# Kernel tuning notes

Hardware: AMD Instinct MI355X
Metric: run time of the kernel (lower is better)

## Reference

```python
import jax, jax.numpy as jnp
from jax import lax
import numpy as np

H = 768          # x_position_dim = num_atoms*3
L = 10           # num_layers
W = 10           # window_size
B = 512          # batch (number of windows)
N_ATOMS = 256


def setup_inputs() -> dict:
    key = jax.random.key(0)
    ks = jax.random.split(key, 9)
    s = 0.02
    return {
        "x_position": jax.random.normal(ks[0], (B, W, N_ATOMS, 3), jnp.float32),
        "fc0_w": jax.random.normal(ks[1], (H, H), jnp.float32) * s,
        "fc0_b": jax.random.normal(ks[2], (H,), jnp.float32) * s,
        "w_ih": jax.random.normal(ks[3], (L, 4 * H, H), jnp.float32) * s,
        "w_hh": jax.random.normal(ks[4], (L, 4 * H, H), jnp.float32) * s,
        "b_ih": jax.random.normal(ks[5], (L, 4 * H), jnp.float32) * s,
        "b_hh": jax.random.normal(ks[6], (L, 4 * H), jnp.float32) * s,
        "fc1_w": jax.random.normal(ks[7], (H, H * W), jnp.float32) * s,
        "fc1_b": jax.random.normal(ks[8], (H,), jnp.float32) * s,
    }


def _lstm_layer(x, wih, whh, bih, bhh):
    # x: (T, B, H). PyTorch gate order: i, f, g, o.
    T, Bb, Hh = x.shape
    # precompute input contribution for all timesteps (one big GEMM)
    gx = jnp.einsum('tbh,gh->tbg', x, wih) + bih + bhh  # (T, B, 4H)

    def step(carry, g_t):
        h, c = carry
        g = g_t + h @ whh.T  # (B, 4H)
        i, f, gg, o = jnp.split(g, 4, axis=-1)
        i = jax.nn.sigmoid(i)
        f = jax.nn.sigmoid(f)
        gg = jnp.tanh(gg)
        o = jax.nn.sigmoid(o)
        c = f * c + i * gg
        h = o * jnp.tanh(c)
        return (h, c), h

    h0 = jnp.zeros((Bb, Hh), x.dtype)
    _, ys = lax.scan(step, (h0, h0), gx)
    return ys  # (T, B, H)


def reference(x_position, fc0_w, fc0_b, w_ih, w_hh, b_ih, b_hh, fc1_w, fc1_b):
    # reshape (B, W, N, 3) -> (B, W, H) -> (W, B, H)
    x = x_position.reshape(-1, W, H)
    x = jnp.swapaxes(x, 0, 1)
    x = x @ fc0_w.T + fc0_b  # fc0
    for l in range(L):
        x = _lstm_layer(x, w_ih[l], w_hh[l], b_ih[l], b_hh[l])
    # (W, B, H) -> (B, W*H) -> fc1 -> (-1, 3)
    xx = jnp.swapaxes(x, 0, 1).reshape(-1, H * W)
    out = xx @ fc1_w.T + fc1_b  # (B, H)
    return out.reshape(-1, 3)
```

## Files before the change

### kernel.cpp

```cpp
#include <hip/hip_runtime.h>

namespace {

using u16 = unsigned short;
typedef short s16x8 __attribute__((ext_vector_type(8)));
typedef float f32x4 __attribute__((ext_vector_type(4)));
typedef u16 u16x4 __attribute__((ext_vector_type(4)));

constexpr int kH  = 768;
constexpr int kW  = 10;
constexpr int kL  = 10;
constexpr int kB  = 512;
constexpr int kG  = 3072;
constexpr int kTB = 5120;
constexpr int kFC1_SPLIT = 12;

__device__ __forceinline__ u16 f2bf(float x) {
  unsigned u = __float_as_uint(x);
  unsigned r = (u + 0x7fffu + ((u >> 16) & 1u)) >> 16;
  return (u16)r;
}
__device__ __forceinline__ float bf2f(u16 h) {
  return __uint_as_float(((unsigned)h) << 16);
}

__device__ __forceinline__ void gl2lds(const void* g, void* l) {
  __builtin_amdgcn_global_load_lds(
      (const __attribute__((address_space(1))) void*)g,
      (__attribute__((address_space(3))) void*)l, 16, 0, 0);
}

__device__ __forceinline__ f32x4 mfma16(s16x8 a, s16x8 b, f32x4 c) {
  return __builtin_amdgcn_mfma_f32_16x16x32_bf16(a, b, c, 0, 0, 0);
}

__device__ __forceinline__ float sigm(float x) { return 1.f / (1.f + __expf(-x)); }

__device__ __forceinline__ int swz_u16(int row, int kc) {
  return row * 32 + ((kc ^ ((row >> 1) & 3)) << 3);
}

__device__ __forceinline__ void split_store(const float4 v, u16* hi, u16* lo, int idx) {
  u16x4 h, l;
  h[0] = f2bf(v.x); l[0] = f2bf(v.x - bf2f(h[0]));
  h[1] = f2bf(v.y); l[1] = f2bf(v.y - bf2f(h[1]));
  h[2] = f2bf(v.z); l[2] = f2bf(v.z - bf2f(h[2]));
  h[3] = f2bf(v.w); l[3] = f2bf(v.w - bf2f(h[3]));
  reinterpret_cast<u16x4*>(hi)[idx] = h;
  reinterpret_cast<u16x4*>(lo)[idx] = l;
}

__global__ __launch_bounds__(256) void split4(const float* __restrict__ in,
                                              u16* __restrict__ hi,
                                              u16* __restrict__ lo) {
  int idx = blockIdx.x * 256 + threadIdx.x;
  split_store(reinterpret_cast<const float4*>(in)[idx], hi, lo, idx);
}

__global__ __launch_bounds__(256) void split2(const float* __restrict__ a,
                                              const float* __restrict__ b,
                                              u16* __restrict__ ahi, u16* __restrict__ alo,
                                              u16* __restrict__ bhi, u16* __restrict__ blo) {
  int idx = blockIdx.x * 256 + threadIdx.x;
  constexpr int half = kG * kH / 4;
  const float* in = a;
  u16 *hi = ahi, *lo = alo;
  if (idx >= half) { in = b; hi = bhi; lo = blo; idx -= half; }
  split_store(reinterpret_cast<const float4*>(in)[idx], hi, lo, idx);
}

__global__ __launch_bounds__(256) void transpose_split(const float* __restrict__ src,
                                                       u16* __restrict__ hi,
                                                       u16* __restrict__ lo) {
  int idx = blockIdx.x * 256 + threadIdx.x;
  int h4 = idx % 192;
  int rest = idx / 192;
  int b = rest % kB;
  int t = rest / kB;
  float4 v = reinterpret_cast<const float4*>(src)[((size_t)b * kW + t) * 192 + h4];
  split_store(v, hi, lo, (int)(((size_t)t * kB + b) * 192 + h4));
}

__global__ __launch_bounds__(256) void pack_sp(const u16* __restrict__ Yhi,
                                               const u16* __restrict__ Ylo,
                                               u16* __restrict__ Xhi,
                                               u16* __restrict__ Xlo) {
  int idx = blockIdx.x * 256 + threadIdx.x;
  int h8 = idx % 96;
  int rest = idx / 96;
  int w = rest % kW;
  int b = rest / kW;
  size_t s = ((size_t)w * kB + b) * 96 + h8;
  size_t d = ((size_t)b * kW + w) * 96 + h8;
  reinterpret_cast<uint4*>(Xhi)[d] = reinterpret_cast<const uint4*>(Yhi)[s];
  reinterpret_cast<uint4*>(Xlo)[d] = reinterpret_cast<const uint4*>(Ylo)[s];
}

template <int BM, int EPI>
__global__ __launch_bounds__(256) void gemm_bf3(
    const u16* __restrict__ Ahi, const u16* __restrict__ Alo,
    const u16* __restrict__ Bhi, const u16* __restrict__ Blo,
    const float* __restrict__ bias1, const float* __restrict__ bias2,
    float* __restrict__ Cf, u16* __restrict__ Chi, u16* __restrict__ Clo,
    int M, int N, int K, int Ksub) {
  constexpr int MR = BM / 64;
  constexpr int WR = BM / 4;
  __shared__ u16 sAh[2][BM * 32], sAl[2][BM * 32];
  __shared__ u16 sBh[2][128 * 32], sBl[2][128 * 32];
  const int tid = threadIdx.x;
  const int wid = tid >> 6;
  const int lane = tid & 63;
  const int bm = blockIdx.y * BM;
  const int bn = blockIdx.x * 128;
  const int kbeg = blockIdx.z * Ksub;

  f32x4 acc[MR][8];
#pragma unroll
  for (int m = 0; m < MR; ++m)
#pragma unroll
    for (int n = 0; n < 8; ++n) acc[m][n] = {0.f, 0.f, 0.f, 0.f};

  const int kc = lane >> 4;
  const int cl = lane & 15;
  const int srow = lane >> 2;
  const int scol = (((lane & 3) ^ ((srow >> 1) & 3)) << 3);

  auto STAGE = [&](int bi, int k0) {
#pragma unroll
    for (int c = 0; c < MR; ++c) {
      int g16 = (wid * MR + c) * 16;
      size_t goff = (size_t)(bm + g16 + srow) * K + k0 + scol;
      gl2lds(Ahi + goff, &sAh[bi][g16 * 32]);
      gl2lds(Alo + goff, &sAl[bi][g16 * 32]);
    }
#pragma unroll
    for (int c = 0; c < 2; ++c) {
      int g16 = (wid * 2 + c) * 16;
      size_t goff = (size_t)(bn + g16 + srow) * K + k0 + scol;
      gl2lds(Bhi + goff, &sBh[bi][g16 * 32]);
      gl2lds(Blo + goff, &sBl[bi][g16 * 32]);
    }
  };

  auto COMPUTE = [&](int bi) {
    s16x8 ah[MR], al[MR];
#pragma unroll
    for (int m = 0; m < MR; ++m) {
      int row = wid * WR + m * 16 + cl;
      ah[m] = *reinterpret_cast<const s16x8*>(&sAh[bi][swz_u16(row, kc)]);
      al[m] = *reinterpret_cast<const s16x8*>(&sAl[bi][swz_u16(row, kc)]);
    }
#pragma unroll
    for (int n = 0; n < 8; ++n) {
      int row = n * 16 + cl;
      s16x8 bh = *reinterpret_cast<const s16x8*>(&sBh[bi][swz_u16(row, kc)]);
      s16x8 bl = *reinterpret_cast<const s16x8*>(&sBl[bi][swz_u16(row, kc)]);
#pragma unroll
      for (int m = 0; m < MR; ++m) acc[m][n] = mfma16(ah[m], bh, acc[m][n]);
#pragma unroll
      for (int m = 0; m < MR; ++m) acc[m][n] = mfma16(ah[m], bl, acc[m][n]);
#pragma unroll
      for (int m = 0; m < MR; ++m) acc[m][n] = mfma16(al[m], bh, acc[m][n]);
    }
  };

  const int NT = Ksub / 32;
  STAGE(0, kbeg);
  int cur = 0;
  for (int t = 0; t < NT - 1; ++t) {
    STAGE(cur ^ 1, kbeg + (t + 1) * 32);
    if constexpr (MR == 2) asm volatile("s_waitcnt vmcnt(8)" ::: "memory");
    else                   asm volatile("s_waitcnt vmcnt(6)" ::: "memory");
    __builtin_amdgcn_s_barrier();
    __builtin_amdgcn_sched_barrier(0);
    COMPUTE(cur);
    __builtin_amdgcn_sched_barrier(0);
    __builtin_amdgcn_s_barrier();
    cur ^= 1;
  }
  asm volatile("s_waitcnt vmcnt(0)" ::: "memory");
  __builtin_amdgcn_s_barrier();
  __builtin_amdgcn_sched_barrier(0);
  COMPUTE(cur);

  const int rq = (lane >> 4) * 4;
#pragma unroll
  for (int m = 0; m < MR; ++m) {
#pragma unroll
    for (int n = 0; n < 8; ++n) {
      int col = bn + n * 16 + cl;
      float badd = (EPI != 3 && bias1) ? bias1[col] : 0.f;
      if (EPI == 2) badd += bias2[col];
#pragma unroll
      for (int q = 0; q < 4; ++q) {
        int row = bm + wid * WR + m * 16 + rq + q;
        float v = acc[m][n][q] + badd;
        if (EPI == 1) {
          size_t off = (size_t)row * N + col;
          u16 h = f2bf(v);
          Chi[off] = h;
          Clo[off] = f2bf(v - bf2f(h));
        } else if (EPI == 3) {
          size_t off = ((size_t)blockIdx.z * M + row) * N + col;
          Cf[off] = v;
        } else {
          Cf[(size_t)row * N + col] = v;
        }
      }
    }
  }
}

__global__ __launch_bounds__(256) void fc1_reduce(const float* __restrict__ part,
                                                  const float* __restrict__ bias,
                                                  float* __restrict__ out) {
  int idx = blockIdx.x * 256 + threadIdx.x;
  float s = bias[idx % kH];
#pragma unroll
  for (int z = 0; z < kFC1_SPLIT; ++z) s += part[(size_t)z * kB * kH + idx];
  out[idx] = s;
}

__global__ __launch_bounds__(256) void lstm_step(
    const u16* __restrict__ Hhi, const u16* __restrict__ Hlo,
    const u16* __restrict__ Whi, const u16* __restrict__ Wlo,
    const float* __restrict__ gxt,
    float* __restrict__ cbuf,
    u16* __restrict__ Ohi, u16* __restrict__ Olo) {
  __shared__ u16 sAh[2][64 * 32], sAl[2][64 * 32];
  __shared__ u16 sBh[2][128 * 32], sBl[2][128 * 32];
  const int tid = threadIdx.x;
  const int wid = tid >> 6;
  const int lane = tid & 63;
  const int u0 = blockIdx.x * 32;
  const int bm = blockIdx.y * 64;

  f32x4 acc[8];
#pragma unroll
  for (int n = 0; n < 8; ++n) acc[n] = {0.f, 0.f, 0.f, 0.f};

  const int kc = lane >> 4;
  const int cl = lane & 15;
  const int srow = lane >> 2;
  const int scol = (((lane & 3) ^ ((srow >> 1) & 3)) << 3);

  auto STAGE = [&](int bi, int k0) {
    {
      int g16 = wid * 16;
      size_t goff = (size_t)(bm + g16 + srow) * kH + k0 + scol;
      gl2lds(Hhi + goff, &sAh[bi][g16 * 32]);
      gl2lds(Hlo + goff, &sAl[bi][g16 * 32]);
    }
#pragma unroll
    for (int c = 0; c < 2; ++c) {
      int g16 = (wid * 2 + c) * 16;
      int slab = g16 >> 5;
      int jb = g16 & 31;
      size_t goff = (size_t)(slab * kH + u0 + jb + srow) * kH + k0 + scol;
      gl2lds(Whi + goff, &sBh[bi][g16 * 32]);
      gl2lds(Wlo + goff, &sBl[bi][g16 * 32]);
    }
  };

  auto COMPUTE = [&](int bi) {
    int arow = wid * 16 + cl;
    s16x8 ah = *reinterpret_cast<const s16x8*>(&sAh[bi][swz_u16(arow, kc)]);
    s16x8 al = *reinterpret_cast<const s16x8*>(&sAl[bi][swz_u16(arow, kc)]);
#pragma unroll
    for (int n = 0; n < 8; ++n) {
      int row = n * 16 + cl;
      s16x8 bh = *reinterpret_cast<const s16x8*>(&sBh[bi][swz_u16(row, kc)]);
      s16x8 bl = *reinterpret_cast<const s16x8*>(&sBl[bi][swz_u16(row, kc)]);
      acc[n] = mfma16(ah, bh, acc[n]);
      acc[n] = mfma16(ah, bl, acc[n]);
      acc[n] = mfma16(al, bh, acc[n]);
    }
  };

  constexpr int NT = kH / 32;
  STAGE(0, 0);
  int cur = 0;
  for (int t = 0; t < NT - 1; ++t) {
    STAGE(cur ^ 1, (t + 1) * 32);
    asm volatile("s_waitcnt vmcnt(6)" ::: "memory");
    __builtin_amdgcn_s_barrier();
    __builtin_amdgcn_sched_barrier(0);
    COMPUTE(cur);
    __builtin_amdgcn_sched_barrier(0);
    __builtin_amdgcn_s_barrier();
    cur ^= 1;
  }
  asm volatile("s_waitcnt vmcnt(0)" ::: "memory");
  __builtin_amdgcn_s_barrier();
  __builtin_amdgcn_sched_barrier(0);
  COMPUTE(cur);

  const int rq = (lane >> 4) * 4;
#pragma unroll
  for (int h = 0; h < 2; ++h) {
    int u = u0 + h * 16 + cl;
#pragma unroll
    for (int q = 0; q < 4; ++q) {
      int r = bm + wid * 16 + rq + q;
      size_t gb = (size_t)r * kG;
      float gi = acc[0 + h][q] + gxt[gb + u];
      float gf = acc[2 + h][q] + gxt[gb + kH + u];
      float gg = acc[4 + h][q] + gxt[gb + 2 * kH + u];
      float go = acc[6 + h][q] + gxt[gb + 3 * kH + u];
      float i_ = sigm(gi), f_ = sigm(gf), g_ = tanhf(gg), o_ = sigm(go);
      size_t co = (size_t)r * kH + u;
      float cn = fmaf(f_, cbuf[co], i_ * g_);
      cbuf[co] = cn;
      float hv = o_ * tanhf(cn);
      u16 hh = f2bf(hv);
      Ohi[co] = hh;
      Olo[co] = f2bf(hv - bf2f(hh));
    }
  }
}

__global__ __launch_bounds__(256) void lstm_t0(const float* __restrict__ gxt,
                                               float* __restrict__ cbuf,
                                               u16* __restrict__ Ohi,
                                               u16* __restrict__ Olo) {
  int idx = blockIdx.x * 256 + threadIdx.x;
  int b = idx / kH, u = idx % kH;
  size_t base = (size_t)b * kG;
  float gi = gxt[base + u];
  float gg = gxt[base + 2 * kH + u];
  float go = gxt[base + 3 * kH + u];
  float i_ = sigm(gi), g_ = tanhf(gg), o_ = sigm(go);
  float cn = i_ * g_;
  cbuf[idx] = cn;
  float hv = o_ * tanhf(cn);
  u16 hh = f2bf(hv);
  Ohi[idx] = hh;
  Olo[idx] = f2bf(hv - bf2f(hh));
}

}

extern "C" void kernel_launch(void* const* d_in, const int* in_sizes, int n_in,
                              void* d_out, int out_size, void* d_ws, size_t ws_size,
                              hipStream_t stream) {
  const float* xpos  = (const float*)d_in[0];
  const float* fc0_w = (const float*)d_in[1];
  const float* fc0_b = (const float*)d_in[2];
  const float* w_ih  = (const float*)d_in[3];
  const float* w_hh  = (const float*)d_in[4];
  const float* b_ih  = (const float*)d_in[5];
  const float* b_hh  = (const float*)d_in[6];
  const float* fc1_w = (const float*)d_in[7];
  const float* fc1_b = (const float*)d_in[8];
  float* out = (float*)d_out;

  char* W = (char*)d_ws;
  float* gx      = (float*)W;
  u16* Xthi      = (u16*)W;
  u16* Xtlo      = Xthi + (size_t)kTB * kH;
  u16* fc1whi    = (u16*)(W + 16777216);
  u16* fc1wlo    = fc1whi + (size_t)kH * kH * kW;
  float* fc1part = (float*)(W + 40370176);
  u16* Yhi       = (u16*)(W + 62914560);
  u16* Ylo       = Yhi + (size_t)kTB * kH;
  float* cbuf    = (float*)(W + 78643200);
  u16* wihhi     = (u16*)(W + 80216064);
  u16* wihlo     = wihhi + (size_t)kG * kH;
  u16* whhhi     = (u16*)(W + 89653248);
  u16* whhlo     = whhhi + (size_t)kG * kH;
  u16* fc0whi    = (u16*)(W + 99090432);
  u16* fc0wlo    = fc0whi + (size_t)kH * kH;

  dim3 blk(256);

  transpose_split<<<3840, blk, 0, stream>>>(xpos, Xthi, Xtlo);
  split4<<<576, blk, 0, stream>>>(fc0_w, fc0whi, fc0wlo);

  gemm_bf3<128, 1><<<dim3(6, 40), blk, 0, stream>>>(
      Xthi, Xtlo, fc0whi, fc0wlo, fc0_b, nullptr, nullptr, Yhi, Ylo,
      kTB, kH, kH, kH);

  for (int l = 0; l < kL; ++l) {
    split2<<<4608, blk, 0, stream>>>(w_ih + (size_t)l * kG * kH,
                                     w_hh + (size_t)l * kG * kH,
                                     wihhi, wihlo, whhhi, whhlo);

    gemm_bf3<128, 2><<<dim3(24, 40), blk, 0, stream>>>(
        Yhi, Ylo, wihhi, wihlo, b_ih + (size_t)l * kG, b_hh + (size_t)l * kG,
        gx, nullptr, nullptr, kTB, kG, kH, kH);

    lstm_t0<<<1536, blk, 0, stream>>>(gx, cbuf, Yhi, Ylo);

    for (int t = 1; t < kW; ++t) {
      lstm_step<<<dim3(24, 8), blk, 0, stream>>>(
          Yhi + (size_t)(t - 1) * kB * kH, Ylo + (size_t)(t - 1) * kB * kH,
          whhhi, whhlo, gx + (size_t)t * kB * kG, cbuf,
          Yhi + (size_t)t * kB * kH, Ylo + (size_t)t * kB * kH);
    }
  }

  split4<<<5760, blk, 0, stream>>>(fc1_w, fc1whi, fc1wlo);
  pack_sp<<<1920, blk, 0, stream>>>(Yhi, Ylo, Xthi, Xtlo);
  gemm_bf3<64, 3><<<dim3(6, 8, kFC1_SPLIT), blk, 0, stream>>>(
      Xthi, Xtlo, fc1whi, fc1wlo, nullptr, nullptr, fc1part, nullptr, nullptr,
      kB, kH, kW * kH, kW * kH / kFC1_SPLIT);
  fc1_reduce<<<1536, blk, 0, stream>>>(fc1part, fc1_b, out);
}
```

Baseline: 3.604 ms.

## Run stacked LSTM as a layer-time wavefront with fused input and recurrent GEMMs

Replaces the per-layer schedule (weight split, big input GEMM, then nine sequential step kernels) with 19 diagonal wavefront launches. Each launch computes every (layer, time) cell on one anti-diagonal, so up to ten layers run concurrently and fill the GPU better. Each cell fuses the input projection and the recurrent projection into a single 48-tile K loop. The fp32 weights are read directly and split into bf16 hi/lo inside the kernel with packed converts, which removes the separate split kernels and the gx buffer. The cost is re-reading and re-converting both weight matrices in every cell instead of once per layer, and the t=0 cells still skip the recurrent half.

```diff
diff --git a/kernel.cpp b/kernel.cpp
--- a/kernel.cpp
+++ b/kernel.cpp
@@ -22,6 +22,11 @@
 }
 __device__ __forceinline__ float bf2f(u16 h) {
   return __uint_as_float(((unsigned)h) << 16);
+}
+__device__ __forceinline__ unsigned cvtpk(float a, float b) {
+  unsigned r;
+  asm("v_cvt_pk_bf16_f32 %0, %1, %2" : "=v"(r) : "v"(a), "v"(b));
+  return r;
 }
 
 __device__ __forceinline__ void gl2lds(const void* g, void* l) {
@@ -54,18 +59,6 @@
                                               u16* __restrict__ hi,
                                               u16* __restrict__ lo) {
   int idx = blockIdx.x * 256 + threadIdx.x;
-  split_store(reinterpret_cast<const float4*>(in)[idx], hi, lo, idx);
-}
-
-__global__ __launch_bounds__(256) void split2(const float* __restrict__ a,
-                                              const float* __restrict__ b,
-                                              u16* __restrict__ ahi, u16* __restrict__ alo,
-                                              u16* __restrict__ bhi, u16* __restrict__ blo) {
-  int idx = blockIdx.x * 256 + threadIdx.x;
-  constexpr int half = kG * kH / 4;
-  const float* in = a;
-  u16 *hi = ahi, *lo = alo;
-  if (idx >= half) { in = b; hi = bhi; lo = blo; idx -= half; }
   split_store(reinterpret_cast<const float4*>(in)[idx], hi, lo, idx);
 }
 
@@ -100,7 +93,7 @@
 __global__ __launch_bounds__(256) void gemm_bf3(
     const u16* __restrict__ Ahi, const u16* __restrict__ Alo,
     const u16* __restrict__ Bhi, const u16* __restrict__ Blo,
-    const float* __restrict__ bias1, const float* __restrict__ bias2,
+    const float* __restrict__ bias1,
     float* __restrict__ Cf, u16* __restrict__ Chi, u16* __restrict__ Clo,
     int M, int N, int K, int Ksub) {
   constexpr int MR = BM / 64;
@@ -190,7 +183,6 @@
     for (int n = 0; n < 8; ++n) {
       int col = bn + n * 16 + cl;
       float badd = (EPI != 3 && bias1) ? bias1[col] : 0.f;
-      if (EPI == 2) badd += bias2[col];
 #pragma unroll
       for (int q = 0; q < 4; ++q) {
         int row = bm + wid * WR + m * 16 + rq + q;
@@ -200,11 +192,9 @@
           u16 h = f2bf(v);
           Chi[off] = h;
           Clo[off] = f2bf(v - bf2f(h));
-        } else if (EPI == 3) {
+        } else {
           size_t off = ((size_t)blockIdx.z * M + row) * N + col;
           Cf[off] = v;
-        } else {
-          Cf[(size_t)row * N + col] = v;
         }
       }
     }
@@ -221,44 +211,88 @@
   out[idx] = s;
 }
 
-__global__ __launch_bounds__(256) void lstm_step(
-    const u16* __restrict__ Hhi, const u16* __restrict__ Hlo,
-    const u16* __restrict__ Whi, const u16* __restrict__ Wlo,
-    const float* __restrict__ gxt,
+__global__ __launch_bounds__(256) void diag_cell(
+    int lmin, int d,
+    u16* __restrict__ fc0Yhi, u16* __restrict__ fc0Ylo,
+    const u16* __restrict__ pHhi, const u16* __restrict__ pHlo,
+    u16* __restrict__ cHhi, u16* __restrict__ cHlo,
     float* __restrict__ cbuf,
-    u16* __restrict__ Ohi, u16* __restrict__ Olo) {
+    const float* __restrict__ w_ih_all, const float* __restrict__ w_hh_all,
+    const float* __restrict__ b_ih_all, const float* __restrict__ b_hh_all) {
+  constexpr int SZ = kB * kH;
   __shared__ u16 sAh[2][64 * 32], sAl[2][64 * 32];
   __shared__ u16 sBh[2][128 * 32], sBl[2][128 * 32];
+
+  const int l = lmin + (int)blockIdx.z;
+  const int t = d - l;
+  const int u0 = blockIdx.x * 32;
+  const int bm = blockIdx.y * 64;
+
+  const u16* hin_hi = (l == 0) ? fc0Yhi + (size_t)t * SZ : pHhi + (size_t)(l - 1) * SZ;
+  const u16* hin_lo = (l == 0) ? fc0Ylo + (size_t)t * SZ : pHlo + (size_t)(l - 1) * SZ;
+  const u16* hpr_hi = pHhi + (size_t)l * SZ;
+  const u16* hpr_lo = pHlo + (size_t)l * SZ;
+  const float* wih = w_ih_all + (size_t)l * kG * kH;
+  const float* whh = w_hh_all + (size_t)l * kG * kH;
+  const float* bih = b_ih_all + (size_t)l * kG;
+  const float* bhh = b_hh_all + (size_t)l * kG;
+
   const int tid = threadIdx.x;
   const int wid = tid >> 6;
   const int lane = tid & 63;
-  const int u0 = blockIdx.x * 32;
-  const int bm = blockIdx.y * 64;
-
-  f32x4 acc[8];
-#pragma unroll
-  for (int n = 0; n < 8; ++n) acc[n] = {0.f, 0.f, 0.f, 0.f};
-
   const int kc = lane >> 4;
   const int cl = lane & 15;
   const int srow = lane >> 2;
   const int scol = (((lane & 3) ^ ((srow >> 1) & 3)) << 3);
 
-  auto STAGE = [&](int bi, int k0) {
-    {
-      int g16 = wid * 16;
-      size_t goff = (size_t)(bm + g16 + srow) * kH + k0 + scol;
-      gl2lds(Hhi + goff, &sAh[bi][g16 * 32]);
-      gl2lds(Hlo + goff, &sAl[bi][g16 * 32]);
-    }
-#pragma unroll
-    for (int c = 0; c < 2; ++c) {
-      int g16 = (wid * 2 + c) * 16;
-      int slab = g16 >> 5;
-      int jb = g16 & 31;
-      size_t goff = (size_t)(slab * kH + u0 + jb + srow) * kH + k0 + scol;
-      gl2lds(Whi + goff, &sBh[bi][g16 * 32]);
-      gl2lds(Wlo + goff, &sBl[bi][g16 * 32]);
+  const int br = tid & 127;
+  const int kh = tid >> 7;
+  const size_t wrowoff = (size_t)((br >> 5) * kH + u0 + (br & 31)) * kH;
+
+  f32x4 acc[8];
+#pragma unroll
+  for (int n = 0; n < 8; ++n) acc[n] = {0.f, 0.f, 0.f, 0.f};
+
+  const int NT = (t == 0) ? 24 : 48;
+  float4 bq0, bq1, bq2, bq3;
+
+  auto ISSUE = [&](int s, int bi) {
+    int ph = s >= 24;
+    int ks = s * 32 - ph * 768;
+    const float* bsrc = (ph ? whh : wih) + wrowoff + ks + kh * 16;
+    bq0 = reinterpret_cast<const float4*>(bsrc)[0];
+    bq1 = reinterpret_cast<const float4*>(bsrc)[1];
+    bq2 = reinterpret_cast<const float4*>(bsrc)[2];
+    bq3 = reinterpret_cast<const float4*>(bsrc)[3];
+    __builtin_amdgcn_sched_barrier(0);
+    const u16* Ah = ph ? hpr_hi : hin_hi;
+    const u16* Al = ph ? hpr_lo : hin_lo;
+    int g16 = wid * 16;
+    size_t goff = (size_t)(bm + g16 + srow) * kH + ks + scol;
+    gl2lds(Ah + goff, &sAh[bi][g16 * 32]);
+    gl2lds(Al + goff, &sAl[bi][g16 * 32]);
+  };
+
+  auto WRITEB = [&](int bi) {
+#pragma unroll
+    for (int half = 0; half < 2; ++half) {
+      float4 a = half ? bq2 : bq0;
+      float4 b = half ? bq3 : bq1;
+      unsigned h0 = cvtpk(a.x, a.y), h1 = cvtpk(a.z, a.w);
+      unsigned h2 = cvtpk(b.x, b.y), h3 = cvtpk(b.z, b.w);
+      float r0 = a.x - __uint_as_float(h0 << 16);
+      float r1 = a.y - __uint_as_float(h0 & 0xffff0000u);
+      float r2 = a.z - __uint_as_float(h1 << 16);
+      float r3 = a.w - __uint_as_float(h1 & 0xffff0000u);
+      float r4 = b.x - __uint_as_float(h2 << 16);
+      float r5 = b.y - __uint_as_float(h2 & 0xffff0000u);
+      float r6 = b.z - __uint_as_float(h3 << 16);
+      float r7 = b.w - __uint_as_float(h3 & 0xffff0000u);
+      unsigned l0 = cvtpk(r0, r1), l1 = cvtpk(r2, r3);
+      unsigned l2 = cvtpk(r4, r5), l3 = cvtpk(r6, r7);
+      int ad = swz_u16(br, kh * 2 + half);
+      reinterpret_cast<uint4&>(sBh[bi][ad]) = uint4{h0, h1, h2, h3};
+      reinterpret_cast<uint4&>(sBl[bi][ad]) = uint4{l0, l1, l2, l3};
     }
   };
 
@@ -277,16 +311,22 @@
     }
   };
 
-  constexpr int NT = kH / 32;
-  STAGE(0, 0);
+  ISSUE(0, 0);
+  asm volatile("s_waitcnt vmcnt(2)" ::: "memory");
+  WRITEB(0);
+  asm volatile("s_waitcnt lgkmcnt(0)" ::: "memory");
+  __builtin_amdgcn_s_barrier();
+
   int cur = 0;
-  for (int t = 0; t < NT - 1; ++t) {
-    STAGE(cur ^ 1, (t + 1) * 32);
-    asm volatile("s_waitcnt vmcnt(6)" ::: "memory");
+  for (int s = 0; s < NT - 1; ++s) {
+    ISSUE(s + 1, cur ^ 1);
+    asm volatile("s_waitcnt vmcnt(2)" ::: "memory");
     __builtin_amdgcn_s_barrier();
     __builtin_amdgcn_sched_barrier(0);
+    WRITEB(cur ^ 1);
     COMPUTE(cur);
     __builtin_amdgcn_sched_barrier(0);
+    asm volatile("s_waitcnt lgkmcnt(0)" ::: "memory");
     __builtin_amdgcn_s_barrier();
     cur ^= 1;
   }
@@ -299,43 +339,34 @@
 #pragma unroll
   for (int h = 0; h < 2; ++h) {
     int u = u0 + h * 16 + cl;
+    float b_i = bih[u] + bhh[u];
+    float b_f = bih[kH + u] + bhh[kH + u];
+    float b_g = bih[2 * kH + u] + bhh[2 * kH + u];
+    float b_o = bih[3 * kH + u] + bhh[3 * kH + u];
 #pragma unroll
     for (int q = 0; q < 4; ++q) {
       int r = bm + wid * 16 + rq + q;
-      size_t gb = (size_t)r * kG;
-      float gi = acc[0 + h][q] + gxt[gb + u];
-      float gf = acc[2 + h][q] + gxt[gb + kH + u];
-      float gg = acc[4 + h][q] + gxt[gb + 2 * kH + u];
-      float go = acc[6 + h][q] + gxt[gb + 3 * kH + u];
+      float gi = acc[0 + h][q] + b_i;
+      float gf = acc[2 + h][q] + b_f;
+      float gg = acc[4 + h][q] + b_g;
+      float go = acc[6 + h][q] + b_o;
       float i_ = sigm(gi), f_ = sigm(gf), g_ = tanhf(gg), o_ = sigm(go);
-      size_t co = (size_t)r * kH + u;
-      float cn = fmaf(f_, cbuf[co], i_ * g_);
+      size_t co = (size_t)l * SZ + (size_t)r * kH + u;
+      float cp = (t == 0) ? 0.f : cbuf[co];
+      float cn = fmaf(f_, cp, i_ * g_);
       cbuf[co] = cn;
       float hv = o_ * tanhf(cn);
-      u16 hh = f2bf(hv);
-      Ohi[co] = hh;
-      Olo[co] = f2bf(hv - bf2f(hh));
+      u16 hh_ = f2bf(hv);
+      u16 hl_ = f2bf(hv - bf2f(hh_));
+      cHhi[co] = hh_;
+      cHlo[co] = hl_;
+      if (l == kL - 1) {
+        size_t yo = (size_t)t * SZ + (size_t)r * kH + u;
+        fc0Yhi[yo] = hh_;
+        fc0Ylo[yo] = hl_;
+      }
     }
   }
-}
-
-__global__ __launch_bounds__(256) void lstm_t0(const float* __restrict__ gxt,
-                                               float* __restrict__ cbuf,
-                                               u16* __restrict__ Ohi,
-                                               u16* __restrict__ Olo) {
-  int idx = blockIdx.x * 256 + threadIdx.x;
-  int b = idx / kH, u = idx % kH;
-  size_t base = (size_t)b * kG;
-  float gi = gxt[base + u];
-  float gg = gxt[base + 2 * kH + u];
-  float go = gxt[base + 3 * kH + u];
-  float i_ = sigm(gi), g_ = tanhf(gg), o_ = sigm(go);
-  float cn = i_ * g_;
-  cbuf[idx] = cn;
-  float hv = o_ * tanhf(cn);
-  u16 hh = f2bf(hv);
-  Ohi[idx] = hh;
-  Olo[idx] = f2bf(hv - bf2f(hh));
 }
 
 }
@@ -355,21 +386,20 @@
   float* out = (float*)d_out;
 
   char* W = (char*)d_ws;
-  float* gx      = (float*)W;
-  u16* Xthi      = (u16*)W;
-  u16* Xtlo      = Xthi + (size_t)kTB * kH;
-  u16* fc1whi    = (u16*)(W + 16777216);
-  u16* fc1wlo    = fc1whi + (size_t)kH * kH * kW;
-  float* fc1part = (float*)(W + 40370176);
-  u16* Yhi       = (u16*)(W + 62914560);
-  u16* Ylo       = Yhi + (size_t)kTB * kH;
-  float* cbuf    = (float*)(W + 78643200);
-  u16* wihhi     = (u16*)(W + 80216064);
-  u16* wihlo     = wihhi + (size_t)kG * kH;
-  u16* whhhi     = (u16*)(W + 89653248);
-  u16* whhlo     = whhhi + (size_t)kG * kH;
-  u16* fc0whi    = (u16*)(W + 99090432);
-  u16* fc0wlo    = fc0whi + (size_t)kH * kH;
+  u16* fc0Yhi = (u16*)W;
+  u16* fc0Ylo = (u16*)(W + 7864320);
+  u16* slotHi[2] = {(u16*)(W + 15728640), (u16*)(W + 31457280)};
+  u16* slotLo[2] = {(u16*)(W + 23592960), (u16*)(W + 39321600)};
+  float* cbuf = (float*)(W + 47185920);
+  u16* Xthi   = (u16*)(W + 15728640);
+  u16* Xtlo   = (u16*)(W + 23592960);
+  u16* fc0whi = (u16*)(W + 62914560);
+  u16* fc0wlo = fc0whi + (size_t)kH * kH;
+  u16* fc1whi = (u16*)(W + 15728640);
+  u16* fc1wlo = (u16*)(W + 27525120);
+  u16* XPhi   = (u16*)(W + 39321600);
+  u16* XPlo   = (u16*)(W + 47185920);
+  float* fc1part = (float*)(W + 62914560);
 
   dim3 blk(256);
 
@@ -377,32 +407,23 @@
   split4<<<576, blk, 0, stream>>>(fc0_w, fc0whi, fc0wlo);
 
   gemm_bf3<128, 1><<<dim3(6, 40), blk, 0, stream>>>(
-      Xthi, Xtlo, fc0whi, fc0wlo, fc0_b, nullptr, nullptr, Yhi, Ylo,
+      Xthi, Xtlo, fc0whi, fc0wlo, fc0_b, nullptr, fc0Yhi, fc0Ylo,
       kTB, kH, kH, kH);
 
-  for (int l = 0; l < kL; ++l) {
-    split2<<<4608, blk, 0, stream>>>(w_ih + (size_t)l * kG * kH,
-                                     w_hh + (size_t)l * kG * kH,
-                                     wihhi, wihlo, whhhi, whhlo);
-
-    gemm_bf3<128, 2><<<dim3(24, 40), blk, 0, stream>>>(
-        Yhi, Ylo, wihhi, wihlo, b_ih + (size_t)l * kG, b_hh + (size_t)l * kG,
-        gx, nullptr, nullptr, kTB, kG, kH, kH);
-
-    lstm_t0<<<1536, blk, 0, stream>>>(gx, cbuf, Yhi, Ylo);
-
-    for (int t = 1; t < kW; ++t) {
-      lstm_step<<<dim3(24, 8), blk, 0, stream>>>(
-          Yhi + (size_t)(t - 1) * kB * kH, Ylo + (size_t)(t - 1) * kB * kH,
-          whhhi, whhlo, gx + (size_t)t * kB * kG, cbuf,
-          Yhi + (size_t)t * kB * kH, Ylo + (size_t)t * kB * kH);
-    }
+  for (int d = 0; d <= 18; ++d) {
+    int lmin = d > 9 ? d - 9 : 0;
+    int lmax = d < 9 ? d : 9;
+    int nc = lmax - lmin + 1;
+    int cs = d & 1, ps = cs ^ 1;
+    diag_cell<<<dim3(24, 8, nc), blk, 0, stream>>>(
+        lmin, d, fc0Yhi, fc0Ylo, slotHi[ps], slotLo[ps], slotHi[cs], slotLo[cs],
+        cbuf, w_ih, w_hh, b_ih, b_hh);
   }
 
   split4<<<5760, blk, 0, stream>>>(fc1_w, fc1whi, fc1wlo);
-  pack_sp<<<1920, blk, 0, stream>>>(Yhi, Ylo, Xthi, Xtlo);
+  pack_sp<<<1920, blk, 0, stream>>>(fc0Yhi, fc0Ylo, XPhi, XPlo);
   gemm_bf3<64, 3><<<dim3(6, 8, kFC1_SPLIT), blk, 0, stream>>>(
-      Xthi, Xtlo, fc1whi, fc1wlo, nullptr, nullptr, fc1part, nullptr, nullptr,
+      XPhi, XPlo, fc1whi, fc1wlo, nullptr, fc1part, nullptr, nullptr,
       kB, kH, kW * kH, kW * kH / kFC1_SPLIT);
   fc1_reduce<<<1536, blk, 0, stream>>>(fc1part, fc1_b, out);
 }
```

Measured after the change: 3.032 ms. 1.19x faster.
